# Kernel tuning notes

Measured on AMD Instinct MI355X. Metric: run time of the kernel, lower is better.

Reference implementation:

```python
import jax, jax.numpy as jnp
import numpy as np

N_NODES = 50000
IN_DIM = 128
HID = 64
HEADS = 4
N_EDGES = 800000


def setup_inputs() -> dict:
    key = jax.random.key(0)
    ks = jax.random.split(key, 16)
    x = jax.random.normal(ks[0], (N_NODES, IN_DIM), dtype=jnp.float32)
    edge_index = jax.random.randint(ks[1], (2, N_EDGES), 0, N_NODES, dtype=jnp.int32)
    s = 0.1
    # layer 0: IN_DIM -> HEADS*HID (concat)
    W0 = jax.random.normal(ks[2], (IN_DIM, HEADS * HID), dtype=jnp.float32) * s
    a_src0 = jax.random.normal(ks[3], (HEADS, HID), dtype=jnp.float32) * s
    a_dst0 = jax.random.normal(ks[4], (HEADS, HID), dtype=jnp.float32) * s
    b0 = jnp.zeros((HEADS * HID,), dtype=jnp.float32)
    # layer 1: HEADS*HID -> HEADS*HID (concat)
    W1 = jax.random.normal(ks[5], (HEADS * HID, HEADS * HID), dtype=jnp.float32) * s
    a_src1 = jax.random.normal(ks[6], (HEADS, HID), dtype=jnp.float32) * s
    a_dst1 = jax.random.normal(ks[7], (HEADS, HID), dtype=jnp.float32) * s
    b1 = jnp.zeros((HEADS * HID,), dtype=jnp.float32)
    # layer 2: HEADS*HID -> HID (heads=1, concat=False)
    W2 = jax.random.normal(ks[8], (HEADS * HID, HID), dtype=jnp.float32) * s
    a_src2 = jax.random.normal(ks[9], (1, HID), dtype=jnp.float32) * s
    a_dst2 = jax.random.normal(ks[10], (1, HID), dtype=jnp.float32) * s
    b2 = jnp.zeros((HID,), dtype=jnp.float32)
    return {"x": x, "edge_index": edge_index,
            "W0": W0, "a_src0": a_src0, "a_dst0": a_dst0, "b0": b0,
            "W1": W1, "a_src1": a_src1, "a_dst1": a_dst1, "b1": b1,
            "W2": W2, "a_src2": a_src2, "a_dst2": a_dst2, "b2": b2}


def gat_conv(h_in, src, dst, W, a_src, a_dst, b, concat):
    """PyG-style GATConv (eval mode, self-loops already appended to src/dst)."""
    H, C = a_src.shape
    n = h_in.shape[0]
    h = (h_in @ W).reshape(n, H, C)                       # [N,H,C]
    alpha_s = jnp.sum(h * a_src[None], axis=-1)            # [N,H]
    alpha_d = jnp.sum(h * a_dst[None], axis=-1)            # [N,H]
    e = jax.nn.leaky_relu(alpha_s[src] + alpha_d[dst], 0.2)  # [E,H]
    # segment softmax over destination neighborhoods (numerically stable)
    m = jax.ops.segment_max(e, dst, num_segments=n)        # [N,H]
    m = jnp.where(jnp.isfinite(m), m, 0.0)
    ex = jnp.exp(e - m[dst])
    denom = jax.ops.segment_sum(ex, dst, num_segments=n)
    alpha = ex / (denom[dst] + 1e-16)                      # [E,H]
    msg = h[src] * alpha[:, :, None]                       # [E,H,C]
    out = jax.ops.segment_sum(msg, dst, num_segments=n)    # [N,H,C]
    out = out.reshape(n, H * C) if concat else out.mean(axis=1)
    return out + b


def reference(x, edge_index, W0, a_src0, a_dst0, b0, W1, a_src1, a_dst1, b1, W2, a_src2, a_dst2, b2):
    n = x.shape[0]
    loops = jnp.arange(n, dtype=edge_index.dtype)
    src = jnp.concatenate([edge_index[0], loops])  # add self-loops (PyG default)
    dst = jnp.concatenate([edge_index[1], loops])
    h = gat_conv(x, src, dst, W0, a_src0, a_dst0, b0, concat=True)
    h = jax.nn.elu(h)
    h = gat_conv(h, src, dst, W1, a_src1, a_dst1, b1, concat=True)
    h = jax.nn.elu(h)
    h = gat_conv(h, src, dst, W2, a_src2, a_dst2, b2, concat=False)
    return h  # [N, HID]
```

## Files before the change

### kernel.cpp

```cpp
#include <hip/hip_runtime.h>
#include <hip/hip_bf16.h>

typedef __hip_bfloat16 bf16;
typedef short s8v __attribute__((ext_vector_type(8)));
typedef float f32x4 __attribute__((ext_vector_type(4)));

__device__ __forceinline__ unsigned short f2bf_bits(float x) {
    union { bf16 h; unsigned short u; } v; v.h = __float2bfloat16(x); return v.u;
}
__device__ __forceinline__ float bfbits2f(unsigned short u) {
    union { unsigned u32; float f; } v; v.u32 = ((unsigned)u) << 16; return v.f;
}

template<typename T>
__device__ __forceinline__ void gload_lds16(const T* g, T* l) {
    __builtin_amdgcn_global_load_lds(
        (const __attribute__((address_space(1))) unsigned int*)g,
        (__attribute__((address_space(3))) unsigned int*)l, 16, 0, 0);
}

__device__ __forceinline__ uint4 load8(const bf16* p) { return *(const uint4*)p; }

__device__ __forceinline__ void tr1(const float* W, bf16* Wt, int idx, int K, int N) {
    int nn = idx / K, k = idx - nn * K;
    Wt[idx] = __float2bfloat16(W[(size_t)k * N + nn]);
}
__global__ void prep_kernel(const float* __restrict__ x, bf16* __restrict__ xb, int nc4,
                            const float* __restrict__ W0, const float* __restrict__ W1,
                            const float* __restrict__ W2, bf16* __restrict__ wt0,
                            bf16* __restrict__ wt1, bf16* __restrict__ wt2,
                            int* __restrict__ cursor, int n) {
    int idx = blockIdx.x * blockDim.x + threadIdx.x;
    if (idx < nc4) {
        float4 f = *(const float4*)(x + (size_t)idx * 4);
        union { uint2 u; unsigned short us[4]; } cv;
        cv.us[0] = f2bf_bits(f.x); cv.us[1] = f2bf_bits(f.y);
        cv.us[2] = f2bf_bits(f.z); cv.us[3] = f2bf_bits(f.w);
        *(uint2*)(xb + (size_t)idx * 4) = cv.u;
        return;
    }
    int i2 = idx - nc4;
    if (i2 < 32768) { tr1(W0, wt0, i2, 128, 256); return; }
    i2 -= 32768;
    if (i2 < 65536) { tr1(W1, wt1, i2, 256, 256); return; }
    i2 -= 65536;
    if (i2 < 16384) { tr1(W2, wt2, i2, 256, 64); return; }
    i2 -= 16384;
    if (i2 < n) cursor[i2] = 0;
}

__global__ void hist_kernel(const int* __restrict__ dst, int* counts, int E, int n) {
    int i = blockIdx.x * blockDim.x + threadIdx.x;
    if (i < E) {
        int d = dst[i];
        if ((unsigned)d < (unsigned)n) atomicAdd(&counts[d], 1);
    }
}

__global__ __launch_bounds__(1024) void scan_phase1(
        const int* __restrict__ counts, int* __restrict__ excl_out,
        int* __restrict__ blocksums, int n) {
    __shared__ int wsum[16];
    __shared__ int woff[16];
    int tid = threadIdx.x, lane = tid & 63, wid = tid >> 6;
    int i = blockIdx.x * 1024 + tid;
    int v = (i < n) ? counts[i] + 1 : 0;
    int incl = v;
    #pragma unroll
    for (int d = 1; d < 64; d <<= 1) {
        int t = __shfl_up(incl, d, 64);
        if (lane >= d) incl += t;
    }
    if (lane == 63) wsum[wid] = incl;
    __syncthreads();
    if (wid == 0) {
        int wv = (lane < 16) ? wsum[lane] : 0;
        int wincl = wv;
        #pragma unroll
        for (int d = 1; d < 16; d <<= 1) {
            int t = __shfl_up(wincl, d, 64);
            if (lane >= d) wincl += t;
        }
        if (lane < 16) woff[lane] = wincl - wv;
    }
    __syncthreads();
    if (i < n) excl_out[i] = woff[wid] + incl - v;
    if (tid == 1023) blocksums[blockIdx.x] = woff[15] + wsum[15];
}

__global__ __launch_bounds__(1024) void scan_phase2(
        const int* __restrict__ blocksums, int* __restrict__ row_ptr,
        int* __restrict__ cursor, int nb, int n) {
    int tid = threadIdx.x, lane = tid & 63;
    int i = blockIdx.x * 1024 + tid;
    int v = (lane < nb) ? blocksums[lane] : 0;
    int incl = v;
    #pragma unroll
    for (int d = 1; d < 64; d <<= 1) {
        int t = __shfl_up(incl, d, 64);
        if (lane >= d) incl += t;
    }
    int excl_lane = incl - v;
    int base = __shfl(excl_lane, blockIdx.x, 64);
    int total = __shfl(incl, nb - 1, 64);
    if (i < n) {
        int val = row_ptr[i] + base;
        row_ptr[i] = val;
        cursor[i] = val;
    }
    if (blockIdx.x == 0 && tid == 0) row_ptr[n] = total;
}

__global__ void scatter_kernel(const int* __restrict__ src, const int* __restrict__ dst,
                               int* cursor, int* col_src, int E, int n) {
    int i = blockIdx.x * blockDim.x + threadIdx.x;
    if (i < E) {
        int d = dst[i];
        if ((unsigned)d >= (unsigned)n) return;
        int s = src[i];
        if ((unsigned)s >= (unsigned)n) s = d;
        int pos = atomicAdd(&cursor[d], 1);
        col_src[pos] = s;
    } else if (i < E + n) {
        int v = i - E;
        int pos = atomicAdd(&cursor[v], 1);
        col_src[pos] = v;
    }
}

__global__ __launch_bounds__(256) void gemm128_kernel(
        const bf16* __restrict__ A, const bf16* __restrict__ Wt, bf16* __restrict__ C,
        const float* __restrict__ a_src, const float* __restrict__ a_dst,
        float* __restrict__ asb, float* __restrict__ adb,
        int M, int K, int N, int H) {
    __shared__ __align__(16) bf16 As[128 * 64];
    __shared__ __align__(16) bf16 Bs[128 * 64];
    int tid = threadIdx.x;
    int w = tid >> 6, l = tid & 63;
    int lm = l & 15, quad = l >> 4;
    int m0 = blockIdx.x * 128, n0 = blockIdx.y * 128;
    int wr = (w >> 1) * 64, wc = (w & 1) * 64;
    int srow = w * 32 + (l >> 3);
    int schunk = l & 7;
    f32x4 acc[4][4] = {};
    for (int kt = 0; kt < K; kt += 64) {
        #pragma unroll
        for (int j = 0; j < 4; ++j) {
            int row = srow + j * 8;
            int g = schunk ^ (row & 7);
            int m = m0 + row; if (m >= M) m = M - 1;
            gload_lds16(A + (size_t)m * K + kt + g * 8, As + row * 64 + schunk * 8);
            gload_lds16(Wt + (size_t)(n0 + row) * K + kt + g * 8, Bs + row * 64 + schunk * 8);
        }
        __syncthreads();
        #pragma unroll
        for (int ks = 0; ks < 2; ++ks) {
            s8v a[4], b[4];
            #pragma unroll
            for (int mi = 0; mi < 4; ++mi) {
                int row = wr + mi * 16 + lm;
                int c = (ks * 4 + quad) ^ (row & 7);
                a[mi] = *(const s8v*)(As + row * 64 + c * 8);
            }
            #pragma unroll
            for (int ni = 0; ni < 4; ++ni) {
                int row = wc + ni * 16 + lm;
                int c = (ks * 4 + quad) ^ (row & 7);
                b[ni] = *(const s8v*)(Bs + row * 64 + c * 8);
            }
            #pragma unroll
            for (int mi = 0; mi < 4; ++mi)
                #pragma unroll
                for (int ni = 0; ni < 4; ++ni)
                    acc[mi][ni] = __builtin_amdgcn_mfma_f32_16x16x32_bf16(
                        a[mi], b[ni], acc[mi][ni], 0, 0, 0);
        }
        __syncthreads();
    }
    int head = (n0 + wc) >> 6;
    float a_s[4], a_d[4];
    #pragma unroll
    for (int ni = 0; ni < 4; ++ni) {
        int col = n0 + wc + ni * 16 + lm;
        a_s[ni] = a_src[col];
        a_d[ni] = a_dst[col];
    }
    #pragma unroll
    for (int mi = 0; mi < 4; ++mi) {
        #pragma unroll
        for (int reg = 0; reg < 4; ++reg) {
            int m = m0 + wr + mi * 16 + quad * 4 + reg;
            float ps = 0.f, pd = 0.f;
            #pragma unroll
            for (int ni = 0; ni < 4; ++ni) {
                float v = acc[mi][ni][reg];
                ps += v * a_s[ni];
                pd += v * a_d[ni];
                if (m < M)
                    C[(size_t)m * N + n0 + wc + ni * 16 + lm] = __float2bfloat16(v);
            }
            #pragma unroll
            for (int d = 1; d < 16; d <<= 1) {
                ps += __shfl_xor(ps, d, 64);
                pd += __shfl_xor(pd, d, 64);
            }
            if (lm == 0 && m < M) {
                asb[(size_t)m * H + head] = ps;
                adb[(size_t)m * H + head] = pd;
            }
        }
    }
}

__global__ __launch_bounds__(256) void gemm64_kernel(
        const bf16* __restrict__ A, const bf16* __restrict__ Wt, bf16* __restrict__ C,
        const float* __restrict__ a_src, const float* __restrict__ a_dst,
        float* __restrict__ asb, float* __restrict__ adb,
        int M, int K, int N) {
    __shared__ __align__(16) bf16 As[64][72];
    __shared__ __align__(16) bf16 Bs[64][72];
    int tid = threadIdx.x;
    int m0 = blockIdx.x * 64;
    int w = tid >> 6;
    int l = tid & 63;
    int lm = l & 15;
    int quad = l >> 4;
    int r = tid >> 2;
    int kb = (tid & 3) * 8;
    f32x4 acc[4] = {};
    int mstage = m0 + r;
    for (int kt = 0; kt < K; kt += 64) {
        #pragma unroll
        for (int c = 0; c < 2; ++c) {
            int kk = kb + c * 32;
            uint4 av = (mstage < M) ? load8(&A[(size_t)mstage * K + kt + kk])
                                    : make_uint4(0, 0, 0, 0);
            *(uint4*)&As[r][kk] = av;
            *(uint4*)&Bs[r][kk] = load8(&Wt[(size_t)r * K + kt + kk]);
        }
        __syncthreads();
        #pragma unroll
        for (int ks = 0; ks < 2; ++ks) {
            s8v a = *(const s8v*)&As[w * 16 + lm][ks * 32 + quad * 8];
            #pragma unroll
            for (int nb = 0; nb < 4; ++nb) {
                s8v b = *(const s8v*)&Bs[nb * 16 + lm][ks * 32 + quad * 8];
                acc[nb] = __builtin_amdgcn_mfma_f32_16x16x32_bf16(a, b, acc[nb], 0, 0, 0);
            }
        }
        __syncthreads();
    }
    float a_s[4], a_d[4];
    #pragma unroll
    for (int nb = 0; nb < 4; ++nb) {
        a_s[nb] = a_src[nb * 16 + lm];
        a_d[nb] = a_dst[nb * 16 + lm];
    }
    #pragma unroll
    for (int reg = 0; reg < 4; ++reg) {
        int m = m0 + w * 16 + quad * 4 + reg;
        float ps = 0.f, pd = 0.f;
        #pragma unroll
        for (int nb = 0; nb < 4; ++nb) {
            float v = acc[nb][reg];
            ps += v * a_s[nb];
            pd += v * a_d[nb];
            if (m < M)
                C[(size_t)m * N + nb * 16 + lm] = __float2bfloat16(v);
        }
        #pragma unroll
        for (int d = 1; d < 16; d <<= 1) {
            ps += __shfl_xor(ps, d, 64);
            pd += __shfl_xor(pd, d, 64);
        }
        if (lm == 0 && m < M) {
            asb[m] = ps;
            adb[m] = pd;
        }
    }
}

__global__ __launch_bounds__(256) void agg4_kernel(
        const bf16* __restrict__ hbuf,
        const float* __restrict__ asb, const float* __restrict__ adb,
        const int* __restrict__ row_ptr, const int* __restrict__ col_src,
        const float* __restrict__ bias,
        bf16* __restrict__ outp, int n) {
    int lane = threadIdx.x & 63;
    int node = blockIdx.x * 4 + (threadIdx.x >> 6);
    if (node >= n) return;
    const int c0 = lane * 4;
    const int head = c0 >> 6;
    int start = row_ptr[node], end = row_ptr[node + 1];
    float adn = adb[(size_t)node * 4 + head];
    float acc[4] = {};
    float denom = 0.f;

    auto edge_w = [&](int s) -> float {
        float x = asb[(size_t)s * 4 + head] + adn;
        x = (x > 0.f) ? x : 0.2f * x;
        return __expf(fminf(x, 30.f));
    };
    auto loadH = [&](int s, float* o) {
        union { uint2 u; unsigned short us[4]; } cv;
        cv.u = *(const uint2*)(hbuf + (size_t)s * 256 + c0);
        #pragma unroll
        for (int v = 0; v < 4; ++v) o[v] = bfbits2f(cv.us[v]);
    };

    int e = start;
    for (; e + 4 <= end; e += 4) {
        int s0 = col_src[e], s1 = col_src[e + 1], s2 = col_src[e + 2], s3 = col_src[e + 3];
        float h0[4], h1[4], h2[4], h3[4];
        loadH(s0, h0); loadH(s1, h1); loadH(s2, h2); loadH(s3, h3);
        float w0 = edge_w(s0), w1 = edge_w(s1), w2 = edge_w(s2), w3 = edge_w(s3);
        denom += (w0 + w1) + (w2 + w3);
        #pragma unroll
        for (int v = 0; v < 4; ++v)
            acc[v] += w0 * h0[v] + w1 * h1[v] + w2 * h2[v] + w3 * h3[v];
    }
    for (; e < end; ++e) {
        int s = col_src[e];
        float hv[4];
        loadH(s, hv);
        float w = edge_w(s);
        denom += w;
        #pragma unroll
        for (int v = 0; v < 4; ++v) acc[v] += w * hv[v];
    }
    float inv = 1.f / (denom + 1e-16f);
    union { uint2 u; unsigned short us[4]; } cv;
    #pragma unroll
    for (int v = 0; v < 4; ++v) {
        float o = acc[v] * inv + bias[c0 + v];
        o = (o > 0.f) ? o : (__expf(o) - 1.f);
        cv.us[v] = f2bf_bits(o);
    }
    *(uint2*)(outp + (size_t)node * 256 + c0) = cv.u;
}

__global__ __launch_bounds__(256) void agg2_kernel(
        const bf16* __restrict__ hbuf,
        const float* __restrict__ asb, const float* __restrict__ adb,
        const int* __restrict__ row_ptr, const int* __restrict__ col_src,
        const float* __restrict__ bias,
        float* __restrict__ outp, int n) {
    int tid = threadIdx.x;
    int l32 = tid & 31;
    int node = blockIdx.x * 8 + (tid >> 5);
    if (node >= n) return;
    const int c0 = l32 * 2;
    int start = row_ptr[node], end = row_ptr[node + 1];
    float adn = adb[node];
    float acc0 = 0.f, acc1 = 0.f, denom = 0.f;

    auto edge_w = [&](int s) -> float {
        float x = asb[s] + adn;
        x = (x > 0.f) ? x : 0.2f * x;
        return __expf(fminf(x, 30.f));
    };
    auto loadH2 = [&](int s, float& o0, float& o1) {
        unsigned u = *(const unsigned*)(hbuf + (size_t)s * 64 + c0);
        o0 = bfbits2f((unsigned short)(u & 0xffffu));
        o1 = bfbits2f((unsigned short)(u >> 16));
    };

    int e = start;
    for (; e + 4 <= end; e += 4) {
        int s0 = col_src[e], s1 = col_src[e + 1], s2 = col_src[e + 2], s3 = col_src[e + 3];
        float a0, b0, a1, b1, a2, b2, a3, b3;
        loadH2(s0, a0, b0); loadH2(s1, a1, b1); loadH2(s2, a2, b2); loadH2(s3, a3, b3);
        float w0 = edge_w(s0), w1 = edge_w(s1), w2 = edge_w(s2), w3 = edge_w(s3);
        denom += (w0 + w1) + (w2 + w3);
        acc0 += w0 * a0 + w1 * a1 + w2 * a2 + w3 * a3;
        acc1 += w0 * b0 + w1 * b1 + w2 * b2 + w3 * b3;
    }
    for (; e < end; ++e) {
        int s = col_src[e];
        float a, b;
        loadH2(s, a, b);
        float w = edge_w(s);
        denom += w;
        acc0 += w * a;
        acc1 += w * b;
    }
    float inv = 1.f / (denom + 1e-16f);
    float2 o;
    o.x = acc0 * inv + bias[c0];
    o.y = acc1 * inv + bias[c0 + 1];
    *(float2*)(outp + (size_t)node * 64 + c0) = o;
}

extern "C" void kernel_launch(void* const* d_in, const int* in_sizes, int n_in,
                              void* d_out, int out_size, void* d_ws, size_t ws_size,
                              hipStream_t stream) {
    const float* x   = (const float*)d_in[0];
    const int*   ei  = (const int*)d_in[1];
    const float* W0  = (const float*)d_in[2];
    const float* as0 = (const float*)d_in[3];
    const float* ad0 = (const float*)d_in[4];
    const float* b0  = (const float*)d_in[5];
    const float* W1  = (const float*)d_in[6];
    const float* as1 = (const float*)d_in[7];
    const float* ad1 = (const float*)d_in[8];
    const float* b1  = (const float*)d_in[9];
    const float* W2  = (const float*)d_in[10];
    const float* as2 = (const float*)d_in[11];
    const float* ad2 = (const float*)d_in[12];
    const float* b2  = (const float*)d_in[13];
    float* out = (float*)d_out;

    const int n = in_sizes[0] / 128;
    const int E = in_sizes[1] / 2;
    const int* esrc = ei;
    const int* edst = ei + E;

    char* ws = (char*)d_ws;
    bf16* hb0 = (bf16*)ws;
    bf16* hb1 = hb0 + (size_t)n * 256;
    bf16* xb  = hb1 + (size_t)n * 256;
    bf16* wt0 = xb + (size_t)n * 128;
    bf16* wt1 = wt0 + 128 * 256;
    bf16* wt2 = wt1 + 256 * 256;
    float* asb = (float*)(wt2 + 256 * 64);
    float* adb = asb + (size_t)n * 4;
    int* row_ptr = (int*)(adb + (size_t)n * 4);
    int* cursor  = row_ptr + (n + 64);
    int* col_src = cursor + n;
    int* blocksums = col_src + (E + n + 64);

    const int nb = (n + 1023) / 1024;
    const int nc4 = n * 128 / 4;

    int prep_threads = nc4 + 114688 + n;
    prep_kernel<<<(prep_threads + 255) / 256, 256, 0, stream>>>(
        x, xb, nc4, W0, W1, W2, wt0, wt1, wt2, cursor, n);
    hist_kernel<<<(E + 255) / 256, 256, 0, stream>>>(edst, cursor, E, n);
    scan_phase1<<<nb, 1024, 0, stream>>>(cursor, row_ptr, blocksums, n);
    scan_phase2<<<nb, 1024, 0, stream>>>(blocksums, row_ptr, cursor, nb, n);
    scatter_kernel<<<(E + n + 255) / 256, 256, 0, stream>>>(esrc, edst, cursor, col_src, E, n);

    dim3 blk(256);
    int mg128 = (n + 127) / 128;
    int mg64  = (n + 63) / 64;
    int ag4 = (n + 3) / 4;
    int ag2 = (n + 7) / 8;

    gemm128_kernel<<<dim3(mg128, 2), blk, 0, stream>>>(xb, wt0, hb0, as0, ad0,
                                                       asb, adb, n, 128, 256, 4);
    agg4_kernel<<<ag4, blk, 0, stream>>>(hb0, asb, adb, row_ptr, col_src, b0, hb1, n);
    gemm128_kernel<<<dim3(mg128, 2), blk, 0, stream>>>(hb1, wt1, hb0, as1, ad1,
                                                       asb, adb, n, 256, 256, 4);
    agg4_kernel<<<ag4, blk, 0, stream>>>(hb0, asb, adb, row_ptr, col_src, b1, hb1, n);
    gemm64_kernel<<<dim3(mg64, 1), blk, 0, stream>>>(hb1, wt2, hb0, as2, ad2,
                                                     asb, adb, n, 256, 64);
    agg2_kernel<<<ag2, blk, 0, stream>>>(hb0, asb, adb, row_ptr, col_src, b2, out, n);
}
```

Before: 408.6 us.

## Fuse CSR build preprocessing into one cooperative kernel with grid syncs

Replaces the five preprocessing launches (convert/transpose, histogram, two scan phases, scatter) with a single cooperative kernel of 256 blocks of 1024 threads that uses grid-stride loops and grid.sync between phases. This removes per-launch overhead and inter-kernel gaps. In exchange it runs with a fixed, possibly smaller grid and adds grid-wide barrier costs, and nb must not exceed 256 (here 49).

```diff
diff --git a/kernel.cpp b/kernel.cpp
--- a/kernel.cpp
+++ b/kernel.cpp
@@ -1,5 +1,8 @@
 #include <hip/hip_runtime.h>
 #include <hip/hip_bf16.h>
+#include <hip/hip_cooperative_groups.h>
+
+namespace cg = cooperative_groups;
 
 typedef __hip_bfloat16 bf16;
 typedef short s8v __attribute__((ext_vector_type(8)));
@@ -25,106 +28,106 @@
     int nn = idx / K, k = idx - nn * K;
     Wt[idx] = __float2bfloat16(W[(size_t)k * N + nn]);
 }
-__global__ void prep_kernel(const float* __restrict__ x, bf16* __restrict__ xb, int nc4,
-                            const float* __restrict__ W0, const float* __restrict__ W1,
-                            const float* __restrict__ W2, bf16* __restrict__ wt0,
-                            bf16* __restrict__ wt1, bf16* __restrict__ wt2,
-                            int* __restrict__ cursor, int n) {
-    int idx = blockIdx.x * blockDim.x + threadIdx.x;
-    if (idx < nc4) {
-        float4 f = *(const float4*)(x + (size_t)idx * 4);
+
+__global__ __launch_bounds__(1024) void build_kernel(
+        const float* __restrict__ x, bf16* __restrict__ xb, int nc4,
+        const float* __restrict__ W0, const float* __restrict__ W1,
+        const float* __restrict__ W2, bf16* __restrict__ wt0,
+        bf16* __restrict__ wt1, bf16* __restrict__ wt2,
+        const int* __restrict__ esrc, const int* __restrict__ edst,
+        int* __restrict__ cursor, int* __restrict__ row_ptr,
+        int* __restrict__ col_src, int* __restrict__ blocksums,
+        int E, int n, int nb) {
+    cg::grid_group grid = cg::this_grid();
+    __shared__ int wsum[16];
+    __shared__ int woff[16];
+    int tid = threadIdx.x;
+    int lane = tid & 63, wid = tid >> 6;
+    int gsize = gridDim.x * blockDim.x;
+    int gtid = blockIdx.x * blockDim.x + tid;
+
+    for (int i = gtid; i < nc4; i += gsize) {
+        float4 f = *(const float4*)(x + (size_t)i * 4);
         union { uint2 u; unsigned short us[4]; } cv;
         cv.us[0] = f2bf_bits(f.x); cv.us[1] = f2bf_bits(f.y);
         cv.us[2] = f2bf_bits(f.z); cv.us[3] = f2bf_bits(f.w);
-        *(uint2*)(xb + (size_t)idx * 4) = cv.u;
-        return;
-    }
-    int i2 = idx - nc4;
-    if (i2 < 32768) { tr1(W0, wt0, i2, 128, 256); return; }
-    i2 -= 32768;
-    if (i2 < 65536) { tr1(W1, wt1, i2, 256, 256); return; }
-    i2 -= 65536;
-    if (i2 < 16384) { tr1(W2, wt2, i2, 256, 64); return; }
-    i2 -= 16384;
-    if (i2 < n) cursor[i2] = 0;
-}
-
-__global__ void hist_kernel(const int* __restrict__ dst, int* counts, int E, int n) {
-    int i = blockIdx.x * blockDim.x + threadIdx.x;
-    if (i < E) {
-        int d = dst[i];
-        if ((unsigned)d < (unsigned)n) atomicAdd(&counts[d], 1);
-    }
-}
-
-__global__ __launch_bounds__(1024) void scan_phase1(
-        const int* __restrict__ counts, int* __restrict__ excl_out,
-        int* __restrict__ blocksums, int n) {
-    __shared__ int wsum[16];
-    __shared__ int woff[16];
-    int tid = threadIdx.x, lane = tid & 63, wid = tid >> 6;
-    int i = blockIdx.x * 1024 + tid;
-    int v = (i < n) ? counts[i] + 1 : 0;
-    int incl = v;
-    #pragma unroll
-    for (int d = 1; d < 64; d <<= 1) {
-        int t = __shfl_up(incl, d, 64);
-        if (lane >= d) incl += t;
-    }
-    if (lane == 63) wsum[wid] = incl;
-    __syncthreads();
-    if (wid == 0) {
-        int wv = (lane < 16) ? wsum[lane] : 0;
-        int wincl = wv;
-        #pragma unroll
-        for (int d = 1; d < 16; d <<= 1) {
-            int t = __shfl_up(wincl, d, 64);
-            if (lane >= d) wincl += t;
-        }
-        if (lane < 16) woff[lane] = wincl - wv;
-    }
-    __syncthreads();
-    if (i < n) excl_out[i] = woff[wid] + incl - v;
-    if (tid == 1023) blocksums[blockIdx.x] = woff[15] + wsum[15];
-}
-
-__global__ __launch_bounds__(1024) void scan_phase2(
-        const int* __restrict__ blocksums, int* __restrict__ row_ptr,
-        int* __restrict__ cursor, int nb, int n) {
-    int tid = threadIdx.x, lane = tid & 63;
-    int i = blockIdx.x * 1024 + tid;
-    int v = (lane < nb) ? blocksums[lane] : 0;
-    int incl = v;
-    #pragma unroll
-    for (int d = 1; d < 64; d <<= 1) {
-        int t = __shfl_up(incl, d, 64);
-        if (lane >= d) incl += t;
-    }
-    int excl_lane = incl - v;
-    int base = __shfl(excl_lane, blockIdx.x, 64);
-    int total = __shfl(incl, nb - 1, 64);
-    if (i < n) {
-        int val = row_ptr[i] + base;
-        row_ptr[i] = val;
-        cursor[i] = val;
-    }
-    if (blockIdx.x == 0 && tid == 0) row_ptr[n] = total;
-}
-
-__global__ void scatter_kernel(const int* __restrict__ src, const int* __restrict__ dst,
-                               int* cursor, int* col_src, int E, int n) {
-    int i = blockIdx.x * blockDim.x + threadIdx.x;
-    if (i < E) {
-        int d = dst[i];
-        if ((unsigned)d >= (unsigned)n) return;
-        int s = src[i];
-        if ((unsigned)s >= (unsigned)n) s = d;
-        int pos = atomicAdd(&cursor[d], 1);
-        col_src[pos] = s;
-    } else if (i < E + n) {
-        int v = i - E;
-        int pos = atomicAdd(&cursor[v], 1);
-        col_src[pos] = v;
+        *(uint2*)(xb + (size_t)i * 4) = cv.u;
+    }
+    for (int i = gtid; i < 114688; i += gsize) {
+        int i2 = i;
+        if (i2 < 32768) tr1(W0, wt0, i2, 128, 256);
+        else if ((i2 -= 32768) < 65536) tr1(W1, wt1, i2, 256, 256);
+        else tr1(W2, wt2, i2 - 65536, 256, 64);
+    }
+    for (int i = gtid; i < n; i += gsize) cursor[i] = 0;
+    grid.sync();
+
+    for (int i = gtid; i < E; i += gsize) {
+        int d = edst[i];
+        if ((unsigned)d < (unsigned)n) atomicAdd(&cursor[d], 1);
+    }
+    grid.sync();
+
+    if (blockIdx.x < (unsigned)nb) {
+        int i = blockIdx.x * 1024 + tid;
+        int v = (i < n) ? cursor[i] + 1 : 0;
+        int incl = v;
+        #pragma unroll
+        for (int d = 1; d < 64; d <<= 1) {
+            int t = __shfl_up(incl, d, 64);
+            if (lane >= d) incl += t;
+        }
+        if (lane == 63) wsum[wid] = incl;
+        __syncthreads();
+        if (wid == 0) {
+            int wv = (lane < 16) ? wsum[lane] : 0;
+            int wincl = wv;
+            #pragma unroll
+            for (int d = 1; d < 16; d <<= 1) {
+                int t = __shfl_up(wincl, d, 64);
+                if (lane >= d) wincl += t;
+            }
+            if (lane < 16) woff[lane] = wincl - wv;
+        }
+        __syncthreads();
+        if (i < n) row_ptr[i] = woff[wid] + incl - v;
+        if (tid == 1023) blocksums[blockIdx.x] = woff[15] + wsum[15];
+    }
+    grid.sync();
+
+    if (blockIdx.x < (unsigned)nb) {
+        int v = (lane < nb) ? blocksums[lane] : 0;
+        int incl = v;
+        #pragma unroll
+        for (int d = 1; d < 64; d <<= 1) {
+            int t = __shfl_up(incl, d, 64);
+            if (lane >= d) incl += t;
+        }
+        int base = __shfl(incl - v, blockIdx.x, 64);
+        int total = __shfl(incl, nb - 1, 64);
+        int i = blockIdx.x * 1024 + tid;
+        if (i < n) {
+            int val = row_ptr[i] + base;
+            row_ptr[i] = val;
+            cursor[i] = val;
+        }
+        if (blockIdx.x == 0 && tid == 0) row_ptr[n] = total;
+    }
+    grid.sync();
+
+    for (int i = gtid; i < E + n; i += gsize) {
+        if (i < E) {
+            int d = edst[i];
+            if ((unsigned)d >= (unsigned)n) continue;
+            int s = esrc[i];
+            if ((unsigned)s >= (unsigned)n) s = d;
+            int pos = atomicAdd(&cursor[d], 1);
+            col_src[pos] = s;
+        } else {
+            int v = i - E;
+            int pos = atomicAdd(&cursor[v], 1);
+            col_src[pos] = v;
+        }
     }
 }
 
@@ -429,16 +432,21 @@
     int* col_src = cursor + n;
     int* blocksums = col_src + (E + n + 64);
 
-    const int nb = (n + 1023) / 1024;
-    const int nc4 = n * 128 / 4;
-
-    int prep_threads = nc4 + 114688 + n;
-    prep_kernel<<<(prep_threads + 255) / 256, 256, 0, stream>>>(
-        x, xb, nc4, W0, W1, W2, wt0, wt1, wt2, cursor, n);
-    hist_kernel<<<(E + 255) / 256, 256, 0, stream>>>(edst, cursor, E, n);
-    scan_phase1<<<nb, 1024, 0, stream>>>(cursor, row_ptr, blocksums, n);
-    scan_phase2<<<nb, 1024, 0, stream>>>(blocksums, row_ptr, cursor, nb, n);
-    scatter_kernel<<<(E + n + 255) / 256, 256, 0, stream>>>(esrc, edst, cursor, col_src, E, n);
+    int nb = (n + 1023) / 1024;
+    int nc4 = n * 128 / 4;
+
+    {
+        void* args[] = {
+            (void*)&x, (void*)&xb, (void*)&nc4,
+            (void*)&W0, (void*)&W1, (void*)&W2,
+            (void*)&wt0, (void*)&wt1, (void*)&wt2,
+            (void*)&esrc, (void*)&edst,
+            (void*)&cursor, (void*)&row_ptr, (void*)&col_src, (void*)&blocksums,
+            (void*)&E, (void*)&n, (void*)&nb
+        };
+        hipLaunchCooperativeKernel((void*)build_kernel, dim3(256), dim3(1024),
+                                   args, 0, stream);
+    }
 
     dim3 blk(256);
     int mg128 = (n + 127) / 128;
```

Result: slower. 552.9 us (+35.3%).
